# Kernel optimization log

Measured on AMD Instinct MI355X. Metric: run time of the kernel, lower is better.

The kernel has to match this reference:

```python
import jax, jax.numpy as jnp
import numpy as np

CHUNK = 128
TAU = 0.7


def setup_inputs() -> dict:
    key = jax.random.key(0)
    ks = jax.random.split(key, 8)
    B, S, D, H, E = 4, 4096, 2048, 1024, 8
    x = jax.random.normal(ks[0], (B, S, D), dtype=jnp.float32)
    prev_expert_indices = jax.random.randint(ks[1], (B,), 0, E)
    # router MLP params (stored as [in, out]); xavier-uniform-like init, zero biases
    def xavier(k, fin, fout):
        lim = np.sqrt(6.0 / (fin + fout)).astype(np.float32)
        return jax.random.uniform(k, (fin, fout), jnp.float32, -lim, lim)
    w1 = xavier(ks[2], D, H)
    b1 = jnp.zeros((H,), jnp.float32)
    w2 = xavier(ks[3], H, H // 2)
    b2 = jnp.zeros((H // 2,), jnp.float32)
    w3 = jax.random.normal(ks[4], (H // 2, E), jnp.float32) * 0.02  # final layer std=0.02
    b3 = jnp.zeros((E,), jnp.float32)
    return {"x": x, "prev_expert_indices": prev_expert_indices,
            "w1": w1, "b1": b1, "w2": w2, "b2": b2, "w3": w3, "b3": b3}


def reference(x, prev_expert_indices, w1, b1, w2, b2, w3, b3):
    B, S, D = x.shape
    E = w3.shape[1]
    C = S // CHUNK  # num_chunks (seq_len divisible by chunk_size)

    # Router MLP on every token (Dropout is identity in eval), then per-chunk mean
    h = jax.nn.relu(x @ w1 + b1)
    h = jax.nn.relu(h @ w2 + b2)
    tok_logits = h @ w3 + b3                                   # [B, S, E]
    chunk_logits = tok_logits.reshape(B, C, CHUNK, E).mean(2)  # [B, C, E]

    top = jnp.argmax(chunk_logits, axis=-1).astype(jnp.int32)  # [B, C]

    # Sequential hysteresis over chunks (prev_expert_indices given => hysteresis active)
    def step(prev, inp):
        logits_c, top_c, is_first = inp  # [B,E], [B], scalar bool
        cur = jnp.take_along_axis(logits_c, top_c[:, None], axis=1)[:, 0]
        pv = jnp.take_along_axis(logits_c, prev[:, None], axis=1)[:, 0]
        switch = (cur - pv) > TAU
        final = jnp.where(is_first, top_c, jnp.where(switch, top_c, prev))
        flips = jnp.where(is_first, 0, switch.sum().astype(jnp.int32))
        return final, (final, flips)

    is_first = jnp.arange(C) == 0
    _, (experts_t, flips_t) = jax.lax.scan(
        step, jnp.zeros((B,), jnp.int32),
        (chunk_logits.transpose(1, 0, 2), top.T, is_first))
    expert_indices = experts_t.T                               # [B, C]

    one_hot = jax.nn.one_hot(expert_indices, E, dtype=jnp.float32)  # [B, C, E]
    routing_weights = jnp.broadcast_to(one_hot[:, :, None, :],
                                       (B, C, CHUNK, E)).reshape(B, S, E)

    # Stats
    probs = jax.nn.softmax(chunk_logits, axis=-1)
    gate_entropy = -(probs * jnp.log(probs + 1e-8)).sum(-1).mean()
    expert_utilization = one_hot.mean((0, 1))                  # [E]
    flip_rate = flips_t.sum().astype(jnp.float32) / (B * max(1, C - 1))
    routing_concentration = jnp.linalg.norm(expert_utilization)

    return (routing_weights, expert_indices, chunk_logits,
            gate_entropy, expert_utilization, flip_rate, routing_concentration)
```

## Files before the change

kernel.cpp:

```cpp
#include <hip/hip_runtime.h>
#include <math.h>

typedef _Float16 half_t;
typedef __attribute__((ext_vector_type(4))) _Float16 half4v;
typedef __attribute__((ext_vector_type(8))) _Float16 half8v;
typedef __attribute__((ext_vector_type(4))) float floatx4;

constexpr int B_ = 4, S_ = 4096, D_ = 2048, H_ = 1024, H2_ = 512, E_ = 8;
constexpr int CHUNK_ = 128;
constexpr int C_ = S_ / CHUNK_;
constexpr int M_ = B_ * S_;
constexpr float TAU_ = 0.7f;
constexpr float WSCALE = 64.0f, OSCALE = 1.0f / 64.0f;

constexpr int OUT_RW = 0;
constexpr int OUT_EI = OUT_RW + B_ * S_ * E_;
constexpr int OUT_CL = OUT_EI + B_ * C_;
constexpr int OUT_GE = OUT_CL + B_ * C_ * E_;
constexpr int OUT_UT = OUT_GE + 1;
constexpr int OUT_FR = OUT_UT + E_;
constexpr int OUT_RC = OUT_FR + 1;

__global__ __launch_bounds__(256)
void prep_kernel(const float* __restrict__ x, const float* __restrict__ w1,
                 const float* __restrict__ w2,
                 half_t* __restrict__ xh, half_t* __restrict__ w1t,
                 half_t* __restrict__ w2th, half_t* __restrict__ w2tl,
                 float* __restrict__ cl_acc)
{
    __shared__ float tile[32][33];
    const int tx = threadIdx.x & 31;
    const int ty = threadIdx.x >> 5;
    const int bid = blockIdx.x;

    if (bid < 8192) {
        const int base = bid * 512 + threadIdx.x;
#pragma unroll
        for (int p = 0; p < 2; ++p) {
            const int j = base + p * 256;
            const float4 a = ((const float4*)x)[2 * j];
            const float4 b = ((const float4*)x)[2 * j + 1];
            half8v h;
            h[0] = (half_t)a.x; h[1] = (half_t)a.y;
            h[2] = (half_t)a.z; h[3] = (half_t)a.w;
            h[4] = (half_t)b.x; h[5] = (half_t)b.y;
            h[6] = (half_t)b.z; h[7] = (half_t)b.w;
            ((half8v*)xh)[j] = h;
        }
    } else if (bid < 10240) {
        const int b2 = bid - 8192;
        const int n0 = (b2 & 31) * 32;
        const int k0 = (b2 >> 5) * 32;
#pragma unroll
        for (int r = 0; r < 4; ++r)
            tile[ty + r * 8][tx] = w1[(size_t)(k0 + ty + r * 8) * H_ + n0 + tx];
        __syncthreads();
#pragma unroll
        for (int r = 0; r < 4; ++r)
            w1t[(size_t)(n0 + ty + r * 8) * D_ + k0 + tx] = (half_t)tile[tx][ty + r * 8];
    } else if (bid < 10752) {
        const int b2 = bid - 10240;
        const int n0 = (b2 & 15) * 32;
        const int k0 = (b2 >> 4) * 32;
#pragma unroll
        for (int r = 0; r < 4; ++r)
            tile[ty + r * 8][tx] = w2[(size_t)(k0 + ty + r * 8) * H2_ + n0 + tx];
        __syncthreads();
#pragma unroll
        for (int r = 0; r < 4; ++r) {
            const float v = tile[tx][ty + r * 8] * WSCALE;
            const half_t h = (half_t)v;
            const size_t off = (size_t)(n0 + ty + r * 8) * H_ + k0 + tx;
            w2th[off] = h;
            w2tl[off] = (half_t)(v - (float)h);
        }
    } else {
        for (int i = threadIdx.x; i < B_ * C_ * E_; i += 256) cl_acc[i] = 0.0f;
    }
}

__device__ __forceinline__ int lds_off_g(int row, int q)
{
    const int line = row >> 1;
    const int sl = (((row & 1) << 2) | q) ^ (line & 7);
    return line * 64 + sl * 8;
}

__device__ __forceinline__ void stage_half_g1(const half_t* __restrict__ g,
                                              half_t* l, int tid)
{
    const int s = tid & 7;
#pragma unroll
    for (int r = 0; r < 2; ++r) {
        const int line = r * 64 + (tid >> 3);
        const int u = s ^ (line & 7);
        const int row = line * 2 + (u >> 2);
        const int kq = (u & 3) * 8;
        __builtin_amdgcn_global_load_lds(
            (const __attribute__((address_space(1))) void*)(g + (size_t)row * D_ + kq),
            (__attribute__((address_space(3))) void*)(l + (r * 512 + tid) * 8),
            16, 0, 0);
    }
}

__global__ __launch_bounds__(512, 2)
void gemm1_kernel(const half_t* __restrict__ Ah,
                  const half_t* __restrict__ BTh,
                  const float* __restrict__ bias, half_t* __restrict__ outh)
{
    constexpr int KD = D_;
    constexpr int ND = H_;
    constexpr int NT = KD / 64;

    __shared__ __align__(16) half_t sA[2][2][256 * 32];
    __shared__ __align__(16) half_t sB[2][2][256 * 32];

    const int tid = threadIdx.x;
    const int lane = tid & 63;
    const int wave = tid >> 6;
    const int wRow = (wave >> 2) * 128;
    const int wCol = (wave & 3) * 64;
    const int fr = lane & 15;
    const int q = lane >> 4;

    const int bid = blockIdx.x;
    const long blockM = (long)((bid & 7) * 8 + (bid >> 5)) * 256;
    const long blockN = (long)((bid >> 3) & 3) * 256;

    const half_t* gA = Ah + (size_t)blockM * KD;
    const half_t* gB = BTh + (size_t)blockN * KD;

    floatx4 acc[8][4];
#pragma unroll
    for (int i = 0; i < 8; ++i)
#pragma unroll
        for (int j = 0; j < 4; ++j) acc[i][j] = (floatx4){0.f, 0.f, 0.f, 0.f};

    stage_half_g1(gA,      sA[0][0], tid);
    stage_half_g1(gB,      sB[0][0], tid);
    stage_half_g1(gA + 32, sA[0][1], tid);
    stage_half_g1(gB + 32, sB[0][1], tid);
    stage_half_g1(gB + 64, sB[1][0], tid);
    stage_half_g1(gA + 64, sA[1][0], tid);
    stage_half_g1(gB + 96, sB[1][1], tid);
    asm volatile("s_waitcnt vmcnt(6)" ::: "memory");
    __builtin_amdgcn_s_barrier();
    __builtin_amdgcn_sched_barrier(0);

    half8v bfr[4];

#define G1_PHASE(BUF, H, MB, STAGE_STMT, TAIL_STMT)                            \
    {                                                                          \
        half8v afr[4];                                                         \
        if ((MB) == 0) {                                                       \
            _Pragma("unroll")                                                  \
            for (int n = 0; n < 4; ++n)                                        \
                bfr[n] = *(const half8v*)(sB[BUF][H] +                         \
                          lds_off_g(wCol + n * 16 + fr, q));                   \
        }                                                                      \
        _Pragma("unroll")                                                      \
        for (int m = 0; m < 4; ++m)                                            \
            afr[m] = *(const half8v*)(sA[BUF][H] +                             \
                      lds_off_g(wRow + (MB) + m * 16 + fr, q));                \
        STAGE_STMT;                                                            \
        __builtin_amdgcn_s_barrier();                                          \
        asm volatile("s_waitcnt lgkmcnt(0)" ::: "memory");                     \
        __builtin_amdgcn_sched_barrier(0);                                     \
        __builtin_amdgcn_s_setprio(1);                                         \
        _Pragma("unroll")                                                      \
        for (int m = 0; m < 4; ++m)                                            \
            _Pragma("unroll")                                                  \
            for (int n = 0; n < 4; ++n)                                        \
                acc[(MB) / 16 + m][n] = __builtin_amdgcn_mfma_f32_16x16x32_f16(\
                    afr[m], bfr[n], acc[(MB) / 16 + m][n], 0, 0, 0);           \
        __builtin_amdgcn_s_setprio(0);                                         \
        TAIL_STMT;                                                             \
        __builtin_amdgcn_s_barrier();                                          \
        __builtin_amdgcn_sched_barrier(0);                                     \
    }

#define G1_TILE(BUF, T)                                                        \
    {                                                                          \
        G1_PHASE(BUF, 0, 0,                                                    \
            if ((T) + 1 < NT)                                                  \
                stage_half_g1(gA + ((T) + 1) * 64 + 32, sA[(BUF) ^ 1][1], tid),\
            );                                                                 \
        G1_PHASE(BUF, 0, 64,                                                   \
            if ((T) + 2 < NT)                                                  \
                stage_half_g1(gB + ((T) + 2) * 64, sB[BUF][0], tid),           \
            );                                                                 \
        G1_PHASE(BUF, 1, 0,                                                    \
            if ((T) + 2 < NT)                                                  \
                stage_half_g1(gA + ((T) + 2) * 64, sA[BUF][0], tid),           \
            );                                                                 \
        G1_PHASE(BUF, 1, 64,                                                   \
            if ((T) + 2 < NT)                                                  \
                stage_half_g1(gB + ((T) + 2) * 64 + 32, sB[BUF][1], tid),      \
            if ((T) < NT - 2) {                                                \
                asm volatile("s_waitcnt vmcnt(6)" ::: "memory");               \
            } else if ((T) == NT - 2) {                                        \
                asm volatile("s_waitcnt vmcnt(0)" ::: "memory");               \
            });                                                                \
    }

#pragma unroll 1
    for (int t = 0; t < NT; t += 2) {
        G1_TILE(0, t);
        G1_TILE(1, t + 1);
    }
#undef G1_TILE
#undef G1_PHASE

    const int orow = (lane >> 4) * 4;
    const int ocol = lane & 15;
#pragma unroll
    for (int n = 0; n < 4; ++n) {
        const long gn = blockN + wCol + n * 16 + ocol;
        const float bj = bias[gn];
#pragma unroll
        for (int m = 0; m < 8; ++m) {
#pragma unroll
            for (int r = 0; r < 4; ++r) {
                const float v = fmaxf(acc[m][n][r] + bj, 0.0f);
                outh[(size_t)(blockM + wRow + m * 16 + orow + r) * ND + gn] = (half_t)v;
            }
        }
    }
}

__global__ __launch_bounds__(256, 3)
void gemm2_fused_kernel(const half_t* __restrict__ Ah,
                        const half_t* __restrict__ BTh, const half_t* __restrict__ BTl,
                        const float* __restrict__ bias, const float* __restrict__ w3,
                        float* __restrict__ cl_acc)
{
    constexpr int KD = H_, BK = 32;
    __shared__ __align__(16) half_t sAh[128 * BK];
    __shared__ __align__(16) half_t sBh[128 * BK];
    __shared__ __align__(16) half_t sBl[128 * BK];

    const int tid = threadIdx.x;
    const int lane = tid & 63;
    const int wave = tid >> 6;
    const int wm = (wave & 1) * 64;
    const int wn = (wave >> 1) * 64;
    const int d = blockIdx.y * 4 + blockIdx.x;
    const int xcd = d & 7;
    const int l = d >> 3;
    const int rowBlk = xcd * 16 + (l >> 2);
    const int colBlk = l & 3;
    const long blockM = (long)rowBlk * 128;
    const long blockN = (long)colBlk * 128;

    floatx4 acc[4][4];
#pragma unroll
    for (int i = 0; i < 4; ++i)
#pragma unroll
        for (int j = 0; j < 4; ++j) acc[i][j] = (floatx4){0.f, 0.f, 0.f, 0.f};

    const int srow = tid >> 2;
    const int skoff = (tid & 3) * 8;
    const int ldsoff = srow * BK + skoff;
    const int fr = lane & 15;
    const int fq = (lane >> 4) * 8;

    for (int k0 = 0; k0 < KD; k0 += BK) {
        __syncthreads();
#pragma unroll
        for (int p = 0; p < 2; ++p) {
            const int row = srow + p * 64;
            const size_t aoff = (size_t)(blockM + row) * KD + k0 + skoff;
            const size_t boff = (size_t)(blockN + row) * KD + k0 + skoff;
            const int loff = ldsoff + p * 2048;
            __builtin_amdgcn_global_load_lds(
                (const __attribute__((address_space(1))) void*)(Ah + aoff),
                (__attribute__((address_space(3))) void*)(sAh + loff), 16, 0, 0);
            __builtin_amdgcn_global_load_lds(
                (const __attribute__((address_space(1))) void*)(BTh + boff),
                (__attribute__((address_space(3))) void*)(sBh + loff), 16, 0, 0);
            __builtin_amdgcn_global_load_lds(
                (const __attribute__((address_space(1))) void*)(BTl + boff),
                (__attribute__((address_space(3))) void*)(sBl + loff), 16, 0, 0);
        }
        __syncthreads();

        half8v fbh[4], fbl[4];
#pragma unroll
        for (int t = 0; t < 4; ++t) {
            fbh[t] = *(const half8v*)(sBh + (wn + t * 16 + fr) * BK + fq);
            fbl[t] = *(const half8v*)(sBl + (wn + t * 16 + fr) * BK + fq);
        }
#pragma unroll
        for (int i = 0; i < 4; ++i) {
            const half8v fah = *(const half8v*)(sAh + (wm + i * 16 + fr) * BK + fq);
#pragma unroll
            for (int j = 0; j < 4; ++j) {
                acc[i][j] = __builtin_amdgcn_mfma_f32_16x16x32_f16(fah, fbh[j], acc[i][j], 0, 0, 0);
                acc[i][j] = __builtin_amdgcn_mfma_f32_16x16x32_f16(fah, fbl[j], acc[i][j], 0, 0, 0);
            }
        }
    }

    const int ocol = lane & 15;
    float p[E_];
#pragma unroll
    for (int e = 0; e < E_; ++e) p[e] = 0.0f;
#pragma unroll
    for (int j = 0; j < 4; ++j) {
        const int gn = (int)blockN + wn + j * 16 + ocol;
        const float bj = bias[gn];
        const float4 w3a = *(const float4*)(w3 + (size_t)gn * E_);
        const float4 w3b = *(const float4*)(w3 + (size_t)gn * E_ + 4);
        float colsum = 0.0f;
#pragma unroll
        for (int i = 0; i < 4; ++i)
#pragma unroll
            for (int r = 0; r < 4; ++r)
                colsum += fmaxf(acc[i][j][r] * OSCALE + bj, 0.0f);
        p[0] += colsum * w3a.x; p[1] += colsum * w3a.y;
        p[2] += colsum * w3a.z; p[3] += colsum * w3a.w;
        p[4] += colsum * w3b.x; p[5] += colsum * w3b.y;
        p[6] += colsum * w3b.z; p[7] += colsum * w3b.w;
    }
#pragma unroll
    for (int e = 0; e < E_; ++e)
#pragma unroll
        for (int off = 32; off > 0; off >>= 1)
            p[e] += __shfl_xor(p[e], off);
#pragma unroll
    for (int e = 0; e < E_; ++e)
        if (lane == e) atomicAdd(&cl_acc[rowBlk * E_ + e], p[e]);
}

__global__ __launch_bounds__(256)
void final_route_kernel(const float* __restrict__ cl_acc, const float* __restrict__ b3,
                        float* __restrict__ out)
{
    __shared__ float cl[B_ * C_][E_];
    __shared__ int tops[B_ * C_];
    __shared__ int finals[B_ * C_];
    __shared__ int flips[B_];
    __shared__ float ent[B_ * C_];

    const int tid = threadIdx.x;

    if (tid < B_ * C_) {
        int best = 0;
        float bvv = -1e30f;
#pragma unroll
        for (int e = 0; e < E_; ++e) {
            const float v = cl_acc[tid * E_ + e] * (1.0f / CHUNK_) + b3[e];
            cl[tid][e] = v;
            if (v > bvv) { bvv = v; best = e; }
        }
        tops[tid] = best;
    }
    __syncthreads();

    if (tid < B_) {
        const int b = tid;
        int prev = 0, fl = 0;
        for (int c = 0; c < C_; ++c) {
            const int t = tops[b * C_ + c];
            int fin;
            if (c == 0) {
                fin = t;
            } else {
                const float cur = cl[b * C_ + c][t];
                const float pv = cl[b * C_ + c][prev];
                const bool sw = (cur - pv) > TAU_;
                if (sw) fl++;
                fin = sw ? t : prev;
            }
            finals[b * C_ + c] = fin;
            prev = fin;
        }
        flips[b] = fl;
    }
    __syncthreads();

    {
        const int tok = blockIdx.x * 256 + tid;
        const int b = tok >> 12;
        const int c = (tok & (S_ - 1)) >> 7;
        const int e = finals[b * C_ + c];
        float4 v0 = make_float4(e == 0 ? 1.f : 0.f, e == 1 ? 1.f : 0.f,
                                e == 2 ? 1.f : 0.f, e == 3 ? 1.f : 0.f);
        float4 v1 = make_float4(e == 4 ? 1.f : 0.f, e == 5 ? 1.f : 0.f,
                                e == 6 ? 1.f : 0.f, e == 7 ? 1.f : 0.f);
        float4* dst = (float4*)(out + OUT_RW + (size_t)tok * E_);
        dst[0] = v0;
        dst[1] = v1;
    }

    if (blockIdx.x == 0) {
        if (tid < B_ * C_) {
            out[OUT_EI + tid] = (float)finals[tid];
#pragma unroll
            for (int e = 0; e < E_; ++e) out[OUT_CL + tid * E_ + e] = cl[tid][e];
            float m = cl[tid][0];
            for (int e = 1; e < E_; ++e) m = fmaxf(m, cl[tid][e]);
            float pr[E_], s = 0.0f;
            for (int e = 0; e < E_; ++e) { pr[e] = expf(cl[tid][e] - m); s += pr[e]; }
            const float inv = 1.0f / s;
            float h = 0.0f;
            for (int e = 0; e < E_; ++e) { const float pe = pr[e] * inv; h -= pe * logf(pe + 1e-8f); }
            ent[tid] = h;
        }
        __syncthreads();
        if (tid == 0) {
            float esum = 0.0f;
            for (int i = 0; i < B_ * C_; ++i) esum += ent[i];
            out[OUT_GE] = esum / (float)(B_ * C_);

            int cnt[E_];
            for (int e = 0; e < E_; ++e) cnt[e] = 0;
            for (int i = 0; i < B_ * C_; ++i) cnt[finals[i]]++;
            float n2 = 0.0f;
            for (int e = 0; e < E_; ++e) {
                const float u = (float)cnt[e] / (float)(B_ * C_);
                out[OUT_UT + e] = u;
                n2 += u * u;
            }
            const int totfl = flips[0] + flips[1] + flips[2] + flips[3];
            out[OUT_FR] = (float)totfl / (float)(B_ * (C_ - 1));
            out[OUT_RC] = sqrtf(n2);
        }
    }
}

extern "C" void kernel_launch(void* const* d_in, const int* in_sizes, int n_in,
                              void* d_out, int out_size, void* d_ws, size_t ws_size,
                              hipStream_t stream)
{
    const float* x  = (const float*)d_in[0];
    const float* w1 = (const float*)d_in[2];
    const float* b1 = (const float*)d_in[3];
    const float* w2 = (const float*)d_in[4];
    const float* b2 = (const float*)d_in[5];
    const float* w3 = (const float*)d_in[6];
    const float* b3 = (const float*)d_in[7];
    float* out = (float*)d_out;

    half_t* xh   = (half_t*)d_ws;
    half_t* w1t  = xh + (size_t)M_ * D_;
    half_t* h1h  = w1t + (size_t)H_ * D_;
    half_t* w2th = h1h + (size_t)M_ * H_;
    half_t* w2tl = w2th + (size_t)H2_ * H_;
    float*  cl_acc = (float*)(w2tl + (size_t)H2_ * H_);

    prep_kernel<<<dim3(10753), dim3(256), 0, stream>>>(x, w1, w2, xh, w1t, w2th, w2tl, cl_acc);
    gemm1_kernel<<<dim3(256), dim3(512), 0, stream>>>(xh, w1t, b1, h1h);
    gemm2_fused_kernel<<<dim3(H2_ / 128, M_ / 128), dim3(256), 0, stream>>>(
        h1h, w2th, w2tl, b2, w3, cl_acc);
    final_route_kernel<<<dim3(M_ / 256), dim3(256), 0, stream>>>(cl_acc, b3, out);
}
```

Before: 342.5 us.

## Drop split-fp16 w2 correction and stage gemm1 epilogue through LDS

Removes the hi/lo fp16 split of w2 and its 64x scaling, so gemm2 runs one MFMA per tile instead of two and loads one B tile instead of two. Rewrites the gemm1 epilogue to write ReLU outputs into a swizzled LDS buffer, reusing the operand shared memory, then store 16-byte vectors to global memory instead of scattered 2-byte stores. Also removes the unroll-1 pragma on the gemm1 main loop. Dropping the low part lowers the precision of the second layer, which can flip argmax or hysteresis decisions near the threshold.

```diff
diff --git a/kernel.cpp b/kernel.cpp
--- a/kernel.cpp
+++ b/kernel.cpp
@@ -11,7 +11,6 @@
 constexpr int C_ = S_ / CHUNK_;
 constexpr int M_ = B_ * S_;
 constexpr float TAU_ = 0.7f;
-constexpr float WSCALE = 64.0f, OSCALE = 1.0f / 64.0f;
 
 constexpr int OUT_RW = 0;
 constexpr int OUT_EI = OUT_RW + B_ * S_ * E_;
@@ -25,7 +24,7 @@
 void prep_kernel(const float* __restrict__ x, const float* __restrict__ w1,
                  const float* __restrict__ w2,
                  half_t* __restrict__ xh, half_t* __restrict__ w1t,
-                 half_t* __restrict__ w2th, half_t* __restrict__ w2tl,
+                 half_t* __restrict__ w2th,
                  float* __restrict__ cl_acc)
 {
     __shared__ float tile[32][33];
@@ -67,13 +66,8 @@
             tile[ty + r * 8][tx] = w2[(size_t)(k0 + ty + r * 8) * H2_ + n0 + tx];
         __syncthreads();
 #pragma unroll
-        for (int r = 0; r < 4; ++r) {
-            const float v = tile[tx][ty + r * 8] * WSCALE;
-            const half_t h = (half_t)v;
-            const size_t off = (size_t)(n0 + ty + r * 8) * H_ + k0 + tx;
-            w2th[off] = h;
-            w2tl[off] = (half_t)(v - (float)h);
-        }
+        for (int r = 0; r < 4; ++r)
+            w2th[(size_t)(n0 + ty + r * 8) * H_ + k0 + tx] = (half_t)tile[tx][ty + r * 8];
     } else {
         for (int i = threadIdx.x; i < B_ * C_ * E_; i += 256) cl_acc[i] = 0.0f;
     }
@@ -112,8 +106,9 @@
     constexpr int ND = H_;
     constexpr int NT = KD / 64;
 
-    __shared__ __align__(16) half_t sA[2][2][256 * 32];
-    __shared__ __align__(16) half_t sB[2][2][256 * 32];
+    __shared__ __align__(16) half_t smem[65536];
+#define SA(BUF, H) (smem + ((BUF) * 2 + (H)) * 8192)
+#define SB(BUF, H) (smem + 32768 + ((BUF) * 2 + (H)) * 8192)
 
     const int tid = threadIdx.x;
     const int lane = tid & 63;
@@ -136,13 +131,13 @@
 #pragma unroll
         for (int j = 0; j < 4; ++j) acc[i][j] = (floatx4){0.f, 0.f, 0.f, 0.f};
 
-    stage_half_g1(gA,      sA[0][0], tid);
-    stage_half_g1(gB,      sB[0][0], tid);
-    stage_half_g1(gA + 32, sA[0][1], tid);
-    stage_half_g1(gB + 32, sB[0][1], tid);
-    stage_half_g1(gB + 64, sB[1][0], tid);
-    stage_half_g1(gA + 64, sA[1][0], tid);
-    stage_half_g1(gB + 96, sB[1][1], tid);
+    stage_half_g1(gA,      SA(0, 0), tid);
+    stage_half_g1(gB,      SB(0, 0), tid);
+    stage_half_g1(gA + 32, SA(0, 1), tid);
+    stage_half_g1(gB + 32, SB(0, 1), tid);
+    stage_half_g1(gB + 64, SB(1, 0), tid);
+    stage_half_g1(gA + 64, SA(1, 0), tid);
+    stage_half_g1(gB + 96, SB(1, 1), tid);
     asm volatile("s_waitcnt vmcnt(6)" ::: "memory");
     __builtin_amdgcn_s_barrier();
     __builtin_amdgcn_sched_barrier(0);
@@ -155,12 +150,12 @@
         if ((MB) == 0) {                                                       \
             _Pragma("unroll")                                                  \
             for (int n = 0; n < 4; ++n)                                        \
-                bfr[n] = *(const half8v*)(sB[BUF][H] +                         \
+                bfr[n] = *(const half8v*)(SB(BUF, H) +                         \
                           lds_off_g(wCol + n * 16 + fr, q));                   \
         }                                                                      \
         _Pragma("unroll")                                                      \
         for (int m = 0; m < 4; ++m)                                            \
-            afr[m] = *(const half8v*)(sA[BUF][H] +                             \
+            afr[m] = *(const half8v*)(SA(BUF, H) +                             \
                       lds_off_g(wRow + (MB) + m * 16 + fr, q));                \
         STAGE_STMT;                                                            \
         __builtin_amdgcn_s_barrier();                                          \
@@ -183,19 +178,19 @@
     {                                                                          \
         G1_PHASE(BUF, 0, 0,                                                    \
             if ((T) + 1 < NT)                                                  \
-                stage_half_g1(gA + ((T) + 1) * 64 + 32, sA[(BUF) ^ 1][1], tid),\
+                stage_half_g1(gA + ((T) + 1) * 64 + 32, SA((BUF) ^ 1, 1), tid),\
             );                                                                 \
         G1_PHASE(BUF, 0, 64,                                                   \
             if ((T) + 2 < NT)                                                  \
-                stage_half_g1(gB + ((T) + 2) * 64, sB[BUF][0], tid),           \
+                stage_half_g1(gB + ((T) + 2) * 64, SB(BUF, 0), tid),           \
             );                                                                 \
         G1_PHASE(BUF, 1, 0,                                                    \
             if ((T) + 2 < NT)                                                  \
-                stage_half_g1(gA + ((T) + 2) * 64, sA[BUF][0], tid),           \
+                stage_half_g1(gA + ((T) + 2) * 64, SA(BUF, 0), tid),           \
             );                                                                 \
         G1_PHASE(BUF, 1, 64,                                                   \
             if ((T) + 2 < NT)                                                  \
-                stage_half_g1(gB + ((T) + 2) * 64 + 32, sB[BUF][1], tid),      \
+                stage_half_g1(gB + ((T) + 2) * 64 + 32, SB(BUF, 1), tid),      \
             if ((T) < NT - 2) {                                                \
                 asm volatile("s_waitcnt vmcnt(6)" ::: "memory");               \
             } else if ((T) == NT - 2) {                                        \
@@ -203,7 +198,6 @@
             });                                                                \
     }
 
-#pragma unroll 1
     for (int t = 0; t < NT; t += 2) {
         G1_TILE(0, t);
         G1_TILE(1, t + 1);
@@ -213,31 +207,52 @@
 
     const int orow = (lane >> 4) * 4;
     const int ocol = lane & 15;
-#pragma unroll
-    for (int n = 0; n < 4; ++n) {
-        const long gn = blockN + wCol + n * 16 + ocol;
-        const float bj = bias[gn];
-#pragma unroll
-        for (int m = 0; m < 8; ++m) {
-#pragma unroll
-            for (int r = 0; r < 4; ++r) {
-                const float v = fmaxf(acc[m][n][r] + bj, 0.0f);
-                outh[(size_t)(blockM + wRow + m * 16 + orow + r) * ND + gn] = (half_t)v;
+    half_t* sC = smem;
+#pragma unroll 1
+    for (int h = 0; h < 2; ++h) {
+        if ((wRow >> 7) == h) {
+#pragma unroll
+            for (int n = 0; n < 4; ++n) {
+                const int col = wCol + n * 16 + ocol;
+                const float bj = bias[blockN + col];
+#pragma unroll
+                for (int m = 0; m < 8; ++m) {
+#pragma unroll
+                    for (int r = 0; r < 4; ++r) {
+                        const int lrow = m * 16 + orow + r;
+                        const int slot = (col >> 3) ^ (((lrow >> 2) & 3) << 3);
+                        sC[lrow * 256 + slot * 8 + (col & 7)] =
+                            (half_t)fmaxf(acc[m][n][r] + bj, 0.0f);
+                    }
+                }
             }
         }
-    }
+        asm volatile("s_waitcnt lgkmcnt(0)" ::: "memory");
+        __builtin_amdgcn_s_barrier();
+#pragma unroll
+        for (int i = 0; i < 8; ++i) {
+            const int g = i * 512 + tid;
+            const int row = g >> 5;
+            const int sl = g & 31;
+            const half8v v = *(const half8v*)(
+                sC + row * 256 + ((sl ^ (((row >> 2) & 3) << 3)) << 3));
+            *(half8v*)(outh + (size_t)(blockM + h * 128 + row) * ND + blockN + sl * 8) = v;
+        }
+        __builtin_amdgcn_s_barrier();
+    }
+#undef SA
+#undef SB
 }
 
 __global__ __launch_bounds__(256, 3)
 void gemm2_fused_kernel(const half_t* __restrict__ Ah,
-                        const half_t* __restrict__ BTh, const half_t* __restrict__ BTl,
+                        const half_t* __restrict__ BTh,
                         const float* __restrict__ bias, const float* __restrict__ w3,
                         float* __restrict__ cl_acc)
 {
     constexpr int KD = H_, BK = 32;
     __shared__ __align__(16) half_t sAh[128 * BK];
     __shared__ __align__(16) half_t sBh[128 * BK];
-    __shared__ __align__(16) half_t sBl[128 * BK];
 
     const int tid = threadIdx.x;
     const int lane = tid & 63;
@@ -278,26 +293,19 @@
             __builtin_amdgcn_global_load_lds(
                 (const __attribute__((address_space(1))) void*)(BTh + boff),
                 (__attribute__((address_space(3))) void*)(sBh + loff), 16, 0, 0);
-            __builtin_amdgcn_global_load_lds(
-                (const __attribute__((address_space(1))) void*)(BTl + boff),
-                (__attribute__((address_space(3))) void*)(sBl + loff), 16, 0, 0);
         }
         __syncthreads();
 
-        half8v fbh[4], fbl[4];
-#pragma unroll
-        for (int t = 0; t < 4; ++t) {
+        half8v fbh[4];
+#pragma unroll
+        for (int t = 0; t < 4; ++t)
             fbh[t] = *(const half8v*)(sBh + (wn + t * 16 + fr) * BK + fq);
-            fbl[t] = *(const half8v*)(sBl + (wn + t * 16 + fr) * BK + fq);
-        }
 #pragma unroll
         for (int i = 0; i < 4; ++i) {
             const half8v fah = *(const half8v*)(sAh + (wm + i * 16 + fr) * BK + fq);
 #pragma unroll
-            for (int j = 0; j < 4; ++j) {
+            for (int j = 0; j < 4; ++j)
                 acc[i][j] = __builtin_amdgcn_mfma_f32_16x16x32_f16(fah, fbh[j], acc[i][j], 0, 0, 0);
-                acc[i][j] = __builtin_amdgcn_mfma_f32_16x16x32_f16(fah, fbl[j], acc[i][j], 0, 0, 0);
-            }
         }
     }
 
@@ -316,7 +324,7 @@
         for (int i = 0; i < 4; ++i)
 #pragma unroll
             for (int r = 0; r < 4; ++r)
-                colsum += fmaxf(acc[i][j][r] * OSCALE + bj, 0.0f);
+                colsum += fmaxf(acc[i][j][r] + bj, 0.0f);
         p[0] += colsum * w3a.x; p[1] += colsum * w3a.y;
         p[2] += colsum * w3a.z; p[3] += colsum * w3a.w;
         p[4] += colsum * w3b.x; p[5] += colsum * w3b.y;
@@ -449,9 +457,9 @@
     half_t* w2tl = w2th + (size_t)H2_ * H_;
     float*  cl_acc = (float*)(w2tl + (size_t)H2_ * H_);
 
-    prep_kernel<<<dim3(10753), dim3(256), 0, stream>>>(x, w1, w2, xh, w1t, w2th, w2tl, cl_acc);
+    prep_kernel<<<dim3(10753), dim3(256), 0, stream>>>(x, w1, w2, xh, w1t, w2th, cl_acc);
     gemm1_kernel<<<dim3(256), dim3(512), 0, stream>>>(xh, w1t, b1, h1h);
     gemm2_fused_kernel<<<dim3(H2_ / 128, M_ / 128), dim3(256), 0, stream>>>(
-        h1h, w2th, w2tl, b2, w3, cl_acc);
+        h1h, w2th, b2, w3, cl_acc);
     final_route_kernel<<<dim3(M_ / 256), dim3(256), 0, stream>>>(cl_acc, b3, out);
 }
```

Result: faster. 323.1 us (-5.6%).
